# Performance work log

Hardware: AMD Instinct MI355X
Metric: run time of the kernel (lower is better)

The kernel has to match this reference:

```python
import jax, jax.numpy as jnp
import numpy as np

C = 768
HEADS = 12

def setup_inputs() -> dict:
    key = jax.random.key(0)
    k1, k2, k3 = jax.random.split(key, 3)
    x = jax.random.normal(k1, (8, C, 32, 32), dtype=jnp.float32)
    # 1x1 convs are channel-wise linear maps; store as [out_c, in_c]
    w_qkv = jax.random.normal(k2, (3 * C, C), dtype=jnp.float32) * (C ** -0.5)
    w_proj = jax.random.normal(k3, (C, C), dtype=jnp.float32) * (C ** -0.5)
    return {"x": x, "w_qkv": w_qkv, "w_proj": w_proj}

def reference(x, w_qkv, w_proj):
    b, c, h, w = x.shape
    heads = HEADS
    dh = c // heads
    n = h * w
    scale = dh ** -0.5
    # 1x1 conv QKV: [b, 3c, h, w] -> [b, 3, heads, dh, n]
    qkv = jnp.einsum('oc,bchw->bohw', w_qkv, x).reshape(b, 3, heads, dh, n)
    q, k, v = qkv[:, 0], qkv[:, 1], qkv[:, 2]  # each [b, heads, dh, n]
    attn = jnp.einsum('bhdn,bhdm->bhnm', q, k) * scale  # [b, heads, n, n]
    attn = jax.nn.softmax(attn, axis=-1)
    out = jnp.einsum('bhnm,bhdm->bhdn', attn, v)  # [b, heads, dh, n]
    out = out.reshape(b, c, h, w)
    return jnp.einsum('oc,bchw->bohw', w_proj, out)
```

## Files before the change

### kernel.cpp

```cpp
#include <hip/hip_runtime.h>

typedef unsigned short u16;
typedef unsigned int u32;
typedef float v4f __attribute__((ext_vector_type(4)));
typedef __bf16 bf16x8 __attribute__((ext_vector_type(8)));

#define BATCH 8
#define CDIM 768
#define NHEAD 12
#define DH 64
#define NSEQ 1024
#define SCL 0.18033688011112042f

__device__ __forceinline__ u16 f2bf(float f) {
  u32 u = __builtin_bit_cast(u32, f);
  u += 0x7fffu + ((u >> 16) & 1u);
  return (u16)(u >> 16);
}

__device__ __forceinline__ u16 b16(float f) {
  return (u16)((__builtin_bit_cast(u32, f) + 0x8000u) >> 16);
}

__device__ __forceinline__ u32 pkbf(float hi, float lo) {
  u32 a = __builtin_bit_cast(u32, hi) + 0x8000u;
  u32 b = __builtin_bit_cast(u32, lo) + 0x8000u;
  return __builtin_amdgcn_perm(a, b, 0x07060302u);
}

__device__ __forceinline__ v4f mfma16(bf16x8 a, bf16x8 b, v4f c) {
  return __builtin_amdgcn_mfma_f32_16x16x32_bf16(a, b, c, 0, 0, 0);
}

__device__ __forceinline__ void gload16(const u16* g, u16* l) {
  __builtin_amdgcn_global_load_lds(
      (const __attribute__((address_space(1))) void*)g,
      (__attribute__((address_space(3))) void*)l, 16, 0, 0);
}

__global__ __launch_bounds__(256) void k_prep(const float* __restrict__ x,
                                              const float* __restrict__ wq,
                                              const float* __restrict__ wp,
                                              u16* __restrict__ xT,
                                              u16* __restrict__ wqb,
                                              u16* __restrict__ wpb) {
  __shared__ u16 Ts[64][72];
  int bid = blockIdx.x;
  int t = threadIdx.x;
  if (bid < 2304) {
    bool isQ = bid < 1728;
    const float* s = isQ ? wq : wp;
    u16* d = isQ ? wqb : wpb;
    int i = (isQ ? bid : bid - 1728) * 256 + t;
    float4 v = ((const float4*)s)[i];
    u32 lo = (u32)f2bf(v.x) | ((u32)f2bf(v.y) << 16);
    u32 hi = (u32)f2bf(v.z) | ((u32)f2bf(v.w) << 16);
    ((uint2*)d)[i] = uint2{lo, hi};
    return;
  }
  int id = bid - 2304;
  int p0 = (id & 15) * 64; id >>= 4;
  int c0 = (id % 12) * 64; int b = id / 12;
  int cr = t >> 4;
  int p4 = (t & 15) * 4;
  const float* src = x + ((size_t)b * CDIM + c0) * NSEQ + p0;
#pragma unroll
  for (int i = 0; i < 4; ++i) {
    int c = cr + i * 16;
    float4 v = *(const float4*)&src[(size_t)c * NSEQ + p4];
    Ts[p4 + 0][c] = f2bf(v.x);
    Ts[p4 + 1][c] = f2bf(v.y);
    Ts[p4 + 2][c] = f2bf(v.z);
    Ts[p4 + 3][c] = f2bf(v.w);
  }
  __syncthreads();
  int p = t >> 2;
  int cq = t & 3;
  u16* dst = xT + ((size_t)b * NSEQ + p0 + p) * CDIM + c0;
#pragma unroll
  for (int j = 0; j < 2; ++j) {
    int ch = cq + j * 4;
    *(int4*)&dst[ch * 8] = *(const int4*)&Ts[p][ch * 8];
  }
}

#define NKT 24

__device__ __forceinline__ void gemm_core(const u16* __restrict__ Ag,
                                          const u16* __restrict__ Bg,
                                          u16* sm, v4f (&acc)[8][4]) {
  int t = threadIdx.x, lane = t & 63, wid = t >> 6;
  int ln = lane & 15, quad = lane >> 4;
  int wm = wid >> 1, wn = wid & 1;

  int srow = wid * 16 + (lane >> 2);
  int scg = ((lane & 3) ^ ((lane >> 3) & 3)) * 8;
  const u16* As0 = Ag + (size_t)srow * CDIM + scg;
  const u16* Bs0 = Bg + (size_t)srow * CDIM + scg;
  int ldw = wid * 512;

  int cA = (quad ^ ((ln >> 1) & 3)) * 8;
  int rA = (wm * 128 + ln) * 32;
  int rB = 8192 + (wn * 64 + ln) * 32;

  {
    u16* sb0 = sm;
    gload16(As0, sb0 + ldw);
    gload16(As0 + (size_t)64 * CDIM, sb0 + 2048 + ldw);
    gload16(As0 + (size_t)128 * CDIM, sb0 + 4096 + ldw);
    gload16(As0 + (size_t)192 * CDIM, sb0 + 6144 + ldw);
    gload16(Bs0, sb0 + 8192 + ldw);
    gload16(Bs0 + (size_t)64 * CDIM, sb0 + 10240 + ldw);
  }
  asm volatile("" ::: "memory");
  {
    u16* sb1 = sm + 12288;
    gload16(As0 + 32, sb1 + ldw);
    gload16(As0 + (size_t)64 * CDIM + 32, sb1 + 2048 + ldw);
    gload16(As0 + (size_t)128 * CDIM + 32, sb1 + 4096 + ldw);
    gload16(As0 + (size_t)192 * CDIM + 32, sb1 + 6144 + ldw);
    gload16(Bs0 + 32, sb1 + 8192 + ldw);
    gload16(Bs0 + (size_t)64 * CDIM + 32, sb1 + 10240 + ldw);
  }
  asm volatile("s_waitcnt vmcnt(6)" ::: "memory");
  asm volatile("s_barrier" ::: "memory");

  for (int kb = 0; kb < 8; ++kb) {
#pragma unroll
    for (int u = 0; u < 3; ++u) {
      int kt = kb * 3 + u;
      const u16* sb = sm + u * 12288;
      u16* nb = sm + ((u + 2) % 3) * 12288;
      int ko = (kt + 2) * 32;

      bf16x8 af[4], bfr[4];
#pragma unroll
      for (int m = 0; m < 4; ++m)
        af[m] = *(const bf16x8*)&sb[rA + m * 512 + cA];
#pragma unroll
      for (int n = 0; n < 4; ++n)
        bfr[n] = *(const bf16x8*)&sb[rB + n * 512 + cA];
      if (kt < NKT - 2) {
        gload16(As0 + ko, nb + ldw);
        gload16(As0 + (size_t)64 * CDIM + ko, nb + 2048 + ldw);
        gload16(Bs0 + ko, nb + 8192 + ldw);
      }
      asm volatile("s_barrier" ::: "memory");
      asm volatile("s_waitcnt lgkmcnt(0)" ::: "memory");
      __builtin_amdgcn_sched_barrier(0);
      __builtin_amdgcn_s_setprio(1);
#pragma unroll
      for (int m = 0; m < 4; ++m)
#pragma unroll
        for (int n = 0; n < 4; ++n)
          acc[m][n] = mfma16(af[m], bfr[n], acc[m][n]);
      __builtin_amdgcn_s_setprio(0);
      asm volatile("s_barrier" ::: "memory");

#pragma unroll
      for (int m = 0; m < 4; ++m)
        af[m] = *(const bf16x8*)&sb[rA + (m + 4) * 512 + cA];
      if (kt < NKT - 2) {
        gload16(As0 + (size_t)128 * CDIM + ko, nb + 4096 + ldw);
        gload16(As0 + (size_t)192 * CDIM + ko, nb + 6144 + ldw);
        gload16(Bs0 + (size_t)64 * CDIM + ko, nb + 10240 + ldw);
        asm volatile("s_waitcnt vmcnt(6)" ::: "memory");
      } else if (kt == NKT - 2) {
        asm volatile("s_waitcnt vmcnt(0)" ::: "memory");
      }
      asm volatile("s_barrier" ::: "memory");
      asm volatile("s_waitcnt lgkmcnt(0)" ::: "memory");
      __builtin_amdgcn_sched_barrier(0);
      __builtin_amdgcn_s_setprio(1);
#pragma unroll
      for (int m = 0; m < 4; ++m)
#pragma unroll
        for (int n = 0; n < 4; ++n)
          acc[m + 4][n] = mfma16(af[m], bfr[n], acc[m + 4][n]);
      __builtin_amdgcn_s_setprio(0);
      asm volatile("s_barrier" ::: "memory");
    }
  }
}

__global__ __launch_bounds__(256, 2) void k_gemm_qkv(const u16* __restrict__ Wb,
                                                     const u16* __restrict__ xT,
                                                     u16* __restrict__ qkT,
                                                     u16* __restrict__ vbuf) {
  __shared__ u16 sm[3 * 12288];
  int bid = blockIdx.x;
  int swz = (bid & 7) * 72 + (bid >> 3);
  int oIdx = swz % 9, pIdx = swz / 9;
  int oT = oIdx * 256;
  int pG = pIdx * 128;

  v4f acc[8][4] = {};
  gemm_core(Wb + (size_t)oT * CDIM, xT + (size_t)pG * CDIM, sm, acc);

  int t = threadIdx.x, lane = t & 63, wid = t >> 6;
  int ln = lane & 15, quad = lane >> 4;
  int wm = wid >> 1, wn = wid & 1;
  bool isV = oT >= 2 * CDIM;
#pragma unroll
  for (int m = 0; m < 8; ++m) {
#pragma unroll
    for (int n = 0; n < 4; ++n) {
      int ro = oT + wm * 128 + m * 16 + quad * 4;
      int cp = pG + wn * 64 + n * 16 + ln;
      int b = cp >> 10, p = cp & 1023;
      if (!isV) {
        u32 lo = (u32)f2bf(acc[m][n][0]) | ((u32)f2bf(acc[m][n][1]) << 16);
        u32 hi = (u32)f2bf(acc[m][n][2]) | ((u32)f2bf(acc[m][n][3]) << 16);
        *(uint2*)&qkT[((size_t)b * NSEQ + p) * 1536 + ro] = uint2{lo, hi};
      } else {
#pragma unroll
        for (int r = 0; r < 4; ++r)
          vbuf[((size_t)b * CDIM + (ro - 2 * CDIM + r)) * NSEQ + p] =
              f2bf(acc[m][n][r]);
      }
    }
  }
}

__global__ __launch_bounds__(256) void k_attn(const u16* __restrict__ qkT,
                                              const u16* __restrict__ vbuf,
                                              u16* __restrict__ attnT) {
  int id = blockIdx.x;
  int b = id & 7;
  int j = id >> 3;
  int h = j % 12;
  int nt0 = (j / 12) * 128;

  int t = threadIdx.x, lane = t & 63, wid = t >> 6;
  int ln = lane & 15, quad = lane >> 4;
  int nbase = nt0 + wid * 32;

  __shared__ u16 Ks[2][64 * 64];
  __shared__ u16 Vs[2][64 * 64];
  __shared__ u16 Pa[4][32 * 72];
  u16* myP = Pa[wid];

  const u16* qbase = qkT + ((size_t)b * NSEQ + nbase) * 1536 + h * DH;
  bf16x8 aq[2][2];
#pragma unroll
  for (int mt = 0; mt < 2; ++mt)
#pragma unroll
    for (int ks = 0; ks < 2; ++ks)
      aq[mt][ks] = *(const bf16x8*)&qbase[(size_t)(mt * 16 + ln) * 1536 + ks * 32 + quad * 8];

  bf16x8 ones;
#pragma unroll
  for (int i = 0; i < 8; ++i) ones[i] = __builtin_bit_cast(__bf16, (u16)0x3F80);

  v4f oacc[2][4] = {};
  v4f lacc[2] = {};

  int sr8 = lane >> 3;
  int sch = ((lane & 7) ^ sr8) * 8;
  const u16* kg0 = qkT + ((size_t)b * NSEQ + wid * 16 + sr8) * 1536 + CDIM + h * DH + sch;
  const u16* vg0 = vbuf + ((size_t)b * CDIM + h * DH + wid * 16 + sr8) * NSEQ + sch;
  int sK = (wid * 16) * 64;

  int sw0 = (quad ^ (ln & 7)) * 8;
  int sw1 = ((4 + quad) ^ (ln & 7)) * 8;

  gload16(kg0, &Ks[0][sK]);
  gload16(kg0 + (size_t)8 * 1536, &Ks[0][sK + 512]);
  gload16(vg0, &Vs[0][sK]);
  gload16(vg0 + 8 * NSEQ, &Vs[0][sK + 512]);
  __syncthreads();

  for (int s = 0; s < 16; ++s) {
    int cur = s & 1, nxt = cur ^ 1;
    if (s < 15) {
      size_t ko = (size_t)(s + 1) * 64 * 1536;
      int vo = (s + 1) * 64;
      gload16(kg0 + ko, &Ks[nxt][sK]);
      gload16(kg0 + ko + (size_t)8 * 1536, &Ks[nxt][sK + 512]);
      gload16(vg0 + vo, &Vs[nxt][sK]);
      gload16(vg0 + vo + 8 * NSEQ, &Vs[nxt][sK + 512]);
    }

#pragma unroll
    for (int ct = 0; ct < 4; ++ct) {
      bf16x8 kf0 = *(const bf16x8*)&Ks[cur][(ct * 16 + ln) * 64 + sw0];
      bf16x8 kf1 = *(const bf16x8*)&Ks[cur][(ct * 16 + ln) * 64 + sw1];
#pragma unroll
      for (int mt = 0; mt < 2; ++mt) {
        v4f sc = {};
        sc = mfma16(kf0, aq[mt][0], sc);
        sc = mfma16(kf1, aq[mt][1], sc);
        float p0 = __builtin_amdgcn_exp2f(sc[0] * SCL);
        float p1 = __builtin_amdgcn_exp2f(sc[1] * SCL);
        float p2 = __builtin_amdgcn_exp2f(sc[2] * SCL);
        float p3 = __builtin_amdgcn_exp2f(sc[3] * SCL);
        *(uint2*)&myP[(mt * 16 + ln) * 72 + ct * 16 + quad * 4] =
            uint2{pkbf(p1, p0), pkbf(p3, p2)};
      }
    }

    bf16x8 ap[2][2];
#pragma unroll
    for (int mt = 0; mt < 2; ++mt)
#pragma unroll
      for (int ks = 0; ks < 2; ++ks)
        ap[mt][ks] = *(const bf16x8*)&myP[(mt * 16 + ln) * 72 + ks * 32 + quad * 8];
#pragma unroll
    for (int mt = 0; mt < 2; ++mt) {
      lacc[mt] = mfma16(ap[mt][0], ones, lacc[mt]);
      lacc[mt] = mfma16(ap[mt][1], ones, lacc[mt]);
    }
#pragma unroll
    for (int nt = 0; nt < 4; ++nt) {
      bf16x8 vf0 = *(const bf16x8*)&Vs[cur][(nt * 16 + ln) * 64 + sw0];
      bf16x8 vf1 = *(const bf16x8*)&Vs[cur][(nt * 16 + ln) * 64 + sw1];
#pragma unroll
      for (int mt = 0; mt < 2; ++mt) {
        oacc[mt][nt] = mfma16(ap[mt][0], vf0, oacc[mt][nt]);
        oacc[mt][nt] = mfma16(ap[mt][1], vf1, oacc[mt][nt]);
      }
    }
    __syncthreads();
  }

#pragma unroll
  for (int mt = 0; mt < 2; ++mt) {
#pragma unroll
    for (int r = 0; r < 4; ++r) {
      float inv = 1.0f / lacc[mt][r];
      int n = nbase + mt * 16 + quad * 4 + r;
      u16* dst = attnT + ((size_t)b * NSEQ + n) * CDIM + h * DH;
#pragma unroll
      for (int nt = 0; nt < 4; ++nt)
        dst[nt * 16 + ln] = b16(oacc[mt][nt][r] * inv);
    }
  }
}

__global__ __launch_bounds__(256, 2) void k_gemm_proj(const u16* __restrict__ Wb,
                                                      const u16* __restrict__ aT,
                                                      float* __restrict__ out) {
  __shared__ u16 sm[3 * 12288];
  int bid = blockIdx.x;
  int swz = (bid & 7) * 24 + (bid >> 3);
  int oIdx = swz % 3, pIdx = swz / 3;
  int oT = oIdx * 256;
  int pG = pIdx * 128;

  v4f acc[8][4] = {};
  gemm_core(Wb + (size_t)oT * CDIM, aT + (size_t)pG * CDIM, sm, acc);

  int t = threadIdx.x, lane = t & 63, wid = t >> 6;
  int ln = lane & 15, quad = lane >> 4;
  int wm = wid >> 1, wn = wid & 1;
#pragma unroll
  for (int m = 0; m < 8; ++m) {
#pragma unroll
    for (int n = 0; n < 4; ++n) {
      int ro = oT + wm * 128 + m * 16 + quad * 4;
      int cp = pG + wn * 64 + n * 16 + ln;
      int b = cp >> 10, p = cp & 1023;
#pragma unroll
      for (int r = 0; r < 4; ++r)
        out[((size_t)b * CDIM + ro + r) * NSEQ + p] = acc[m][n][r];
    }
  }
}

extern "C" void kernel_launch(void* const* d_in, const int* in_sizes, int n_in,
                              void* d_out, int out_size, void* d_ws, size_t ws_size,
                              hipStream_t stream) {
  const float* x = (const float*)d_in[0];
  const float* w_qkv = (const float*)d_in[1];
  const float* w_proj = (const float*)d_in[2];
  float* out = (float*)d_out;

  char* ws = (char*)d_ws;
  u16* wqkv_bf = (u16*)(ws);
  u16* wproj_bf = (u16*)(ws + 3538944);
  u16* xT = (u16*)(ws + 4718592);
  u16* vbuf = (u16*)(ws + 17301504);
  u16* qkT = (u16*)d_out;
  u16* attnT = xT;

  k_prep<<<dim3(3840), dim3(256), 0, stream>>>(x, w_qkv, w_proj, xT, wqkv_bf, wproj_bf);
  k_gemm_qkv<<<dim3(576), dim3(256), 0, stream>>>(wqkv_bf, xT, qkT, vbuf);
  k_attn<<<dim3(768), dim3(256), 0, stream>>>(qkT, vbuf, attnT);
  k_gemm_proj<<<dim3(192), dim3(256), 0, stream>>>(wproj_bf, attnT, out);
}
```

Measured before the change: 184.6 us.

## Enlarge GEMM tiles to 256x256 with 8 waves and double-buffered 64-wide K stages

The shared QKV/projection GEMM core moves from a 256x128 tile with 4 waves and a triple-buffered 32-wide K pipeline to a 256x256 tile with 8 waves. It now double-buffers 64-wide K stages (two 32-wide sub-slabs each) and interleaves the global-to-LDS loads with MFMA phases through new macros. The goal is more data reuse per loaded tile and fewer K iterations. The cost is 128KB of LDS per block, which allows at most one block per CU. Grid sizes halve to 288 and 96 blocks, so the projection GEMM may leave many CUs idle.

```diff
diff --git a/kernel.cpp b/kernel.cpp
--- a/kernel.cpp
+++ b/kernel.cpp
@@ -84,122 +84,97 @@
   }
 }
 
-#define NKT 24
+#define NIT 6
+
+#define STAGE(gp, db, isB, ks, kt) do {                                   \
+    u16* Ld_ = sm + (db) * 32768 + (isB) * 16384 + (ks) * 8192 + ldw;     \
+    const u16* Gp_ = (gp) + (size_t)(kt) * 64 + (ks) * 32;                \
+    gload16(Gp_, Ld_);                                                    \
+    gload16(Gp_ + (size_t)128 * CDIM, Ld_ + 4096);                        \
+  } while (0)
+
+#define PHASE(db, ks, mh, ...) do {                                       \
+    const u16* Ab_ = sm + (db) * 32768 + (ks) * 8192;                     \
+    const u16* Bb_ = Ab_ + 16384;                                         \
+    bf16x8 af[4];                                                         \
+    _Pragma("unroll") for (int m = 0; m < 4; ++m)                         \
+      af[m] = *(const bf16x8*)&Ab_[rAr + (mh) * 2048 + m * 512 + slot];   \
+    if ((mh) == 0) {                                                      \
+      _Pragma("unroll") for (int n = 0; n < 4; ++n)                       \
+        bfr[n] = *(const bf16x8*)&Bb_[rBr + n * 512 + slot];              \
+    }                                                                     \
+    __VA_ARGS__;                                                          \
+    asm volatile("s_barrier" ::: "memory");                               \
+    asm volatile("s_waitcnt lgkmcnt(0)" ::: "memory");                    \
+    __builtin_amdgcn_sched_barrier(0);                                    \
+    __builtin_amdgcn_s_setprio(1);                                        \
+    _Pragma("unroll") for (int m = 0; m < 4; ++m)                         \
+      _Pragma("unroll") for (int n = 0; n < 4; ++n)                       \
+        acc[(mh) * 4 + m][n] = mfma16(af[m], bfr[n], acc[(mh) * 4 + m][n]); \
+    __builtin_amdgcn_s_setprio(0);                                        \
+    __builtin_amdgcn_sched_barrier(0);                                    \
+    asm volatile("s_barrier" ::: "memory");                               \
+  } while (0)
+
+#define VM4 asm volatile("s_waitcnt vmcnt(4)" ::: "memory")
+#define VM0 asm volatile("s_waitcnt vmcnt(0)" ::: "memory")
+#define FEN asm volatile("" ::: "memory")
 
 __device__ __forceinline__ void gemm_core(const u16* __restrict__ Ag,
                                           const u16* __restrict__ Bg,
                                           u16* sm, v4f (&acc)[8][4]) {
   int t = threadIdx.x, lane = t & 63, wid = t >> 6;
   int ln = lane & 15, quad = lane >> 4;
-  int wm = wid >> 1, wn = wid & 1;
-
-  int srow = wid * 16 + (lane >> 2);
-  int scg = ((lane & 3) ^ ((lane >> 3) & 3)) * 8;
-  const u16* As0 = Ag + (size_t)srow * CDIM + scg;
-  const u16* Bs0 = Bg + (size_t)srow * CDIM + scg;
+  int wm = wid >> 2, wn = wid & 3;
+
+  const u16* As = Ag + (size_t)(t >> 2) * CDIM + ((t & 3) ^ ((t >> 3) & 3)) * 8;
+  const u16* Bs = Bg + (size_t)(t >> 2) * CDIM + ((t & 3) ^ ((t >> 3) & 3)) * 8;
   int ldw = wid * 512;
 
-  int cA = (quad ^ ((ln >> 1) & 3)) * 8;
-  int rA = (wm * 128 + ln) * 32;
-  int rB = 8192 + (wn * 64 + ln) * 32;
-
-  {
-    u16* sb0 = sm;
-    gload16(As0, sb0 + ldw);
-    gload16(As0 + (size_t)64 * CDIM, sb0 + 2048 + ldw);
-    gload16(As0 + (size_t)128 * CDIM, sb0 + 4096 + ldw);
-    gload16(As0 + (size_t)192 * CDIM, sb0 + 6144 + ldw);
-    gload16(Bs0, sb0 + 8192 + ldw);
-    gload16(Bs0 + (size_t)64 * CDIM, sb0 + 10240 + ldw);
-  }
-  asm volatile("" ::: "memory");
-  {
-    u16* sb1 = sm + 12288;
-    gload16(As0 + 32, sb1 + ldw);
-    gload16(As0 + (size_t)64 * CDIM + 32, sb1 + 2048 + ldw);
-    gload16(As0 + (size_t)128 * CDIM + 32, sb1 + 4096 + ldw);
-    gload16(As0 + (size_t)192 * CDIM + 32, sb1 + 6144 + ldw);
-    gload16(Bs0 + 32, sb1 + 8192 + ldw);
-    gload16(Bs0 + (size_t)64 * CDIM + 32, sb1 + 10240 + ldw);
-  }
-  asm volatile("s_waitcnt vmcnt(6)" ::: "memory");
+  int slot = (quad ^ ((ln >> 1) & 3)) * 8;
+  int rAr = (wm * 128 + ln) * 32;
+  int rBr = (wn * 64 + ln) * 32;
+
+  bf16x8 bfr[4];
+
+  STAGE(As, 0, 0, 0, 0); FEN;
+  STAGE(Bs, 0, 1, 0, 0); FEN;
+  STAGE(As, 0, 0, 1, 0); FEN;
+  STAGE(Bs, 0, 1, 1, 0);
+  VM4;
   asm volatile("s_barrier" ::: "memory");
 
-  for (int kb = 0; kb < 8; ++kb) {
-#pragma unroll
-    for (int u = 0; u < 3; ++u) {
-      int kt = kb * 3 + u;
-      const u16* sb = sm + u * 12288;
-      u16* nb = sm + ((u + 2) % 3) * 12288;
-      int ko = (kt + 2) * 32;
-
-      bf16x8 af[4], bfr[4];
-#pragma unroll
-      for (int m = 0; m < 4; ++m)
-        af[m] = *(const bf16x8*)&sb[rA + m * 512 + cA];
-#pragma unroll
-      for (int n = 0; n < 4; ++n)
-        bfr[n] = *(const bf16x8*)&sb[rB + n * 512 + cA];
-      if (kt < NKT - 2) {
-        gload16(As0 + ko, nb + ldw);
-        gload16(As0 + (size_t)64 * CDIM + ko, nb + 2048 + ldw);
-        gload16(Bs0 + ko, nb + 8192 + ldw);
-      }
-      asm volatile("s_barrier" ::: "memory");
-      asm volatile("s_waitcnt lgkmcnt(0)" ::: "memory");
-      __builtin_amdgcn_sched_barrier(0);
-      __builtin_amdgcn_s_setprio(1);
-#pragma unroll
-      for (int m = 0; m < 4; ++m)
-#pragma unroll
-        for (int n = 0; n < 4; ++n)
-          acc[m][n] = mfma16(af[m], bfr[n], acc[m][n]);
-      __builtin_amdgcn_s_setprio(0);
-      asm volatile("s_barrier" ::: "memory");
-
-#pragma unroll
-      for (int m = 0; m < 4; ++m)
-        af[m] = *(const bf16x8*)&sb[rA + (m + 4) * 512 + cA];
-      if (kt < NKT - 2) {
-        gload16(As0 + (size_t)128 * CDIM + ko, nb + 4096 + ldw);
-        gload16(As0 + (size_t)192 * CDIM + ko, nb + 6144 + ldw);
-        gload16(Bs0 + (size_t)64 * CDIM + ko, nb + 10240 + ldw);
-        asm volatile("s_waitcnt vmcnt(6)" ::: "memory");
-      } else if (kt == NKT - 2) {
-        asm volatile("s_waitcnt vmcnt(0)" ::: "memory");
-      }
-      asm volatile("s_barrier" ::: "memory");
-      asm volatile("s_waitcnt lgkmcnt(0)" ::: "memory");
-      __builtin_amdgcn_sched_barrier(0);
-      __builtin_amdgcn_s_setprio(1);
-#pragma unroll
-      for (int m = 0; m < 4; ++m)
-#pragma unroll
-        for (int n = 0; n < 4; ++n)
-          acc[m + 4][n] = mfma16(af[m], bfr[n], acc[m + 4][n]);
-      __builtin_amdgcn_s_setprio(0);
-      asm volatile("s_barrier" ::: "memory");
-    }
-  }
-}
-
-__global__ __launch_bounds__(256, 2) void k_gemm_qkv(const u16* __restrict__ Wb,
+  for (int i = 0; i < NIT; ++i) {
+    int b = 2 * i + 1, n2 = 2 * i + 2;
+    bool nl = (i < NIT - 1);
+    PHASE(0, 0, 0, STAGE(As, 1, 0, 0, b));
+    PHASE(0, 0, 1, STAGE(Bs, 1, 1, 0, b); VM4);
+    PHASE(0, 1, 0, STAGE(As, 1, 0, 1, b));
+    PHASE(0, 1, 1, STAGE(Bs, 1, 1, 1, b); VM4);
+    PHASE(1, 0, 0, if (nl) STAGE(As, 0, 0, 0, n2));
+    PHASE(1, 0, 1, if (nl) { STAGE(Bs, 0, 1, 0, n2); VM4; } else { VM0; });
+    PHASE(1, 1, 0, if (nl) STAGE(As, 0, 0, 1, n2));
+    PHASE(1, 1, 1, if (nl) { STAGE(Bs, 0, 1, 1, n2); VM4; });
+  }
+}
+
+__global__ __launch_bounds__(512, 2) void k_gemm_qkv(const u16* __restrict__ Wb,
                                                      const u16* __restrict__ xT,
                                                      u16* __restrict__ qkT,
                                                      u16* __restrict__ vbuf) {
-  __shared__ u16 sm[3 * 12288];
+  __shared__ u16 sm[65536];
   int bid = blockIdx.x;
-  int swz = (bid & 7) * 72 + (bid >> 3);
+  int swz = (bid & 7) * 36 + (bid >> 3);
   int oIdx = swz % 9, pIdx = swz / 9;
   int oT = oIdx * 256;
-  int pG = pIdx * 128;
+  int pG = pIdx * 256;
 
   v4f acc[8][4] = {};
   gemm_core(Wb + (size_t)oT * CDIM, xT + (size_t)pG * CDIM, sm, acc);
 
   int t = threadIdx.x, lane = t & 63, wid = t >> 6;
   int ln = lane & 15, quad = lane >> 4;
-  int wm = wid >> 1, wn = wid & 1;
+  int wm = wid >> 2, wn = wid & 3;
   bool isV = oT >= 2 * CDIM;
 #pragma unroll
   for (int m = 0; m < 8; ++m) {
@@ -337,22 +312,22 @@
   }
 }
 
-__global__ __launch_bounds__(256, 2) void k_gemm_proj(const u16* __restrict__ Wb,
+__global__ __launch_bounds__(512, 2) void k_gemm_proj(const u16* __restrict__ Wb,
                                                       const u16* __restrict__ aT,
                                                       float* __restrict__ out) {
-  __shared__ u16 sm[3 * 12288];
+  __shared__ u16 sm[65536];
   int bid = blockIdx.x;
-  int swz = (bid & 7) * 24 + (bid >> 3);
+  int swz = (bid & 7) * 12 + (bid >> 3);
   int oIdx = swz % 3, pIdx = swz / 3;
   int oT = oIdx * 256;
-  int pG = pIdx * 128;
+  int pG = pIdx * 256;
 
   v4f acc[8][4] = {};
   gemm_core(Wb + (size_t)oT * CDIM, aT + (size_t)pG * CDIM, sm, acc);
 
   int t = threadIdx.x, lane = t & 63, wid = t >> 6;
   int ln = lane & 15, quad = lane >> 4;
-  int wm = wid >> 1, wn = wid & 1;
+  int wm = wid >> 2, wn = wid & 3;
 #pragma unroll
   for (int m = 0; m < 8; ++m) {
 #pragma unroll
@@ -384,7 +359,7 @@
   u16* attnT = xT;
 
   k_prep<<<dim3(3840), dim3(256), 0, stream>>>(x, w_qkv, w_proj, xT, wqkv_bf, wproj_bf);
-  k_gemm_qkv<<<dim3(576), dim3(256), 0, stream>>>(wqkv_bf, xT, qkT, vbuf);
+  k_gemm_qkv<<<dim3(288), dim3(512), 0, stream>>>(wqkv_bf, xT, qkT, vbuf);
   k_attn<<<dim3(768), dim3(256), 0, stream>>>(qkT, vbuf, attnT);
-  k_gemm_proj<<<dim3(192), dim3(256), 0, stream>>>(wproj_bf, attnT, out);
-}
+  k_gemm_proj<<<dim3(96), dim3(512), 0, stream>>>(wproj_bf, attnT, out);
+}
```

Measured after the change: 198.0 us. 7.3% more time.

## Switch GEMM core to double-buffered LDS and raise occupancy to 3 blocks

Applied to the files above, without the earlier changes.

Replaces the triple-buffered shared-memory pipeline in the shared GEMM core with a double-buffered one that prefetches one k-tile ahead, and rebalances which tile rows are loaded in each half-iteration. The reduced LDS footprint lets launch bounds rise to three blocks per CU for the QKV and projection GEMMs. This trades prefetch depth for occupancy, which may expose more memory latency and tightens the register budget for the large accumulator array.

```diff
diff --git a/kernel.cpp b/kernel.cpp
--- a/kernel.cpp
+++ b/kernel.cpp
@@ -104,90 +104,81 @@
   int rB = 8192 + (wn * 64 + ln) * 32;
 
   {
-    u16* sb0 = sm;
-    gload16(As0, sb0 + ldw);
-    gload16(As0 + (size_t)64 * CDIM, sb0 + 2048 + ldw);
-    gload16(As0 + (size_t)128 * CDIM, sb0 + 4096 + ldw);
-    gload16(As0 + (size_t)192 * CDIM, sb0 + 6144 + ldw);
-    gload16(Bs0, sb0 + 8192 + ldw);
-    gload16(Bs0 + (size_t)64 * CDIM, sb0 + 10240 + ldw);
+    u16* s0 = sm;
+    gload16(As0, s0 + ldw);
+    gload16(As0 + (size_t)128 * CDIM, s0 + 4096 + ldw);
+    gload16(Bs0, s0 + 8192 + ldw);
+    gload16(Bs0 + (size_t)64 * CDIM, s0 + 10240 + ldw);
   }
   asm volatile("" ::: "memory");
   {
-    u16* sb1 = sm + 12288;
-    gload16(As0 + 32, sb1 + ldw);
-    gload16(As0 + (size_t)64 * CDIM + 32, sb1 + 2048 + ldw);
-    gload16(As0 + (size_t)128 * CDIM + 32, sb1 + 4096 + ldw);
-    gload16(As0 + (size_t)192 * CDIM + 32, sb1 + 6144 + ldw);
-    gload16(Bs0 + 32, sb1 + 8192 + ldw);
-    gload16(Bs0 + (size_t)64 * CDIM + 32, sb1 + 10240 + ldw);
-  }
-  asm volatile("s_waitcnt vmcnt(6)" ::: "memory");
+    u16* s0 = sm;
+    gload16(As0 + (size_t)64 * CDIM, s0 + 2048 + ldw);
+    gload16(As0 + (size_t)192 * CDIM, s0 + 6144 + ldw);
+  }
+  asm volatile("s_waitcnt vmcnt(2)" ::: "memory");
   asm volatile("s_barrier" ::: "memory");
 
-  for (int kb = 0; kb < 8; ++kb) {
-#pragma unroll
-    for (int u = 0; u < 3; ++u) {
-      int kt = kb * 3 + u;
-      const u16* sb = sm + u * 12288;
-      u16* nb = sm + ((u + 2) % 3) * 12288;
-      int ko = (kt + 2) * 32;
-
-      bf16x8 af[4], bfr[4];
-#pragma unroll
-      for (int m = 0; m < 4; ++m)
-        af[m] = *(const bf16x8*)&sb[rA + m * 512 + cA];
+  for (int kt = 0; kt < NKT; ++kt) {
+    const u16* sb = sm + (kt & 1) * 12288;
+    u16* nb = sm + ((kt + 1) & 1) * 12288;
+    int ko = (kt + 1) * 32;
+
+    bf16x8 af[4], bfr[4];
+#pragma unroll
+    for (int m = 0; m < 4; ++m)
+      af[m] = *(const bf16x8*)&sb[rA + m * 512 + cA];
+#pragma unroll
+    for (int n = 0; n < 4; ++n)
+      bfr[n] = *(const bf16x8*)&sb[rB + n * 512 + cA];
+    if (kt < NKT - 1) {
+      gload16(As0 + ko, nb + ldw);
+      gload16(As0 + (size_t)128 * CDIM + ko, nb + 4096 + ldw);
+      gload16(Bs0 + ko, nb + 8192 + ldw);
+      gload16(Bs0 + (size_t)64 * CDIM + ko, nb + 10240 + ldw);
+      asm volatile("s_waitcnt vmcnt(4)" ::: "memory");
+    } else {
+      asm volatile("s_waitcnt vmcnt(0)" ::: "memory");
+    }
+    asm volatile("s_barrier" ::: "memory");
+    asm volatile("s_waitcnt lgkmcnt(0)" ::: "memory");
+    __builtin_amdgcn_sched_barrier(0);
+    __builtin_amdgcn_s_setprio(1);
+#pragma unroll
+    for (int m = 0; m < 4; ++m)
 #pragma unroll
       for (int n = 0; n < 4; ++n)
-        bfr[n] = *(const bf16x8*)&sb[rB + n * 512 + cA];
-      if (kt < NKT - 2) {
-        gload16(As0 + ko, nb + ldw);
-        gload16(As0 + (size_t)64 * CDIM + ko, nb + 2048 + ldw);
-        gload16(Bs0 + ko, nb + 8192 + ldw);
-      }
-      asm volatile("s_barrier" ::: "memory");
-      asm volatile("s_waitcnt lgkmcnt(0)" ::: "memory");
-      __builtin_amdgcn_sched_barrier(0);
-      __builtin_amdgcn_s_setprio(1);
-#pragma unroll
-      for (int m = 0; m < 4; ++m)
-#pragma unroll
-        for (int n = 0; n < 4; ++n)
-          acc[m][n] = mfma16(af[m], bfr[n], acc[m][n]);
-      __builtin_amdgcn_s_setprio(0);
-      asm volatile("s_barrier" ::: "memory");
-
-#pragma unroll
-      for (int m = 0; m < 4; ++m)
-        af[m] = *(const bf16x8*)&sb[rA + (m + 4) * 512 + cA];
-      if (kt < NKT - 2) {
-        gload16(As0 + (size_t)128 * CDIM + ko, nb + 4096 + ldw);
-        gload16(As0 + (size_t)192 * CDIM + ko, nb + 6144 + ldw);
-        gload16(Bs0 + (size_t)64 * CDIM + ko, nb + 10240 + ldw);
-        asm volatile("s_waitcnt vmcnt(6)" ::: "memory");
-      } else if (kt == NKT - 2) {
-        asm volatile("s_waitcnt vmcnt(0)" ::: "memory");
-      }
-      asm volatile("s_barrier" ::: "memory");
-      asm volatile("s_waitcnt lgkmcnt(0)" ::: "memory");
-      __builtin_amdgcn_sched_barrier(0);
-      __builtin_amdgcn_s_setprio(1);
-#pragma unroll
-      for (int m = 0; m < 4; ++m)
-#pragma unroll
-        for (int n = 0; n < 4; ++n)
-          acc[m + 4][n] = mfma16(af[m], bfr[n], acc[m + 4][n]);
-      __builtin_amdgcn_s_setprio(0);
-      asm volatile("s_barrier" ::: "memory");
-    }
-  }
-}
-
-__global__ __launch_bounds__(256, 2) void k_gemm_qkv(const u16* __restrict__ Wb,
+        acc[m][n] = mfma16(af[m], bfr[n], acc[m][n]);
+    __builtin_amdgcn_s_setprio(0);
+    asm volatile("s_barrier" ::: "memory");
+
+#pragma unroll
+    for (int m = 0; m < 4; ++m)
+      af[m] = *(const bf16x8*)&sb[rA + (m + 4) * 512 + cA];
+    if (kt < NKT - 1) {
+      gload16(As0 + (size_t)64 * CDIM + ko, nb + 2048 + ldw);
+      gload16(As0 + (size_t)192 * CDIM + ko, nb + 6144 + ldw);
+      asm volatile("s_waitcnt vmcnt(2)" ::: "memory");
+    }
+    asm volatile("s_barrier" ::: "memory");
+    asm volatile("s_waitcnt lgkmcnt(0)" ::: "memory");
+    __builtin_amdgcn_sched_barrier(0);
+    __builtin_amdgcn_s_setprio(1);
+#pragma unroll
+    for (int m = 0; m < 4; ++m)
+#pragma unroll
+      for (int n = 0; n < 4; ++n)
+        acc[m + 4][n] = mfma16(af[m], bfr[n], acc[m + 4][n]);
+    __builtin_amdgcn_s_setprio(0);
+    asm volatile("s_barrier" ::: "memory");
+  }
+}
+
+__global__ __launch_bounds__(256, 3) void k_gemm_qkv(const u16* __restrict__ Wb,
                                                      const u16* __restrict__ xT,
                                                      u16* __restrict__ qkT,
                                                      u16* __restrict__ vbuf) {
-  __shared__ u16 sm[3 * 12288];
+  __shared__ u16 sm[2 * 12288];
   int bid = blockIdx.x;
   int swz = (bid & 7) * 72 + (bid >> 3);
   int oIdx = swz % 9, pIdx = swz / 9;
@@ -337,10 +328,10 @@
   }
 }
 
-__global__ __launch_bounds__(256, 2) void k_gemm_proj(const u16* __restrict__ Wb,
+__global__ __launch_bounds__(256, 3) void k_gemm_proj(const u16* __restrict__ Wb,
                                                       const u16* __restrict__ aT,
                                                       float* __restrict__ out) {
-  __shared__ u16 sm[3 * 12288];
+  __shared__ u16 sm[2 * 12288];
   int bid = blockIdx.x;
   int swz = (bid & 7) * 24 + (bid >> 3);
   int oIdx = swz % 3, pIdx = swz / 3;
```

Result: slower. 218.7 us (+18.5%).

## Retile QKV GEMM to 288x256 tiles with 8 waves and 256 blocks

Applied to the files above, without the earlier changes.

Replaces the QKV projection GEMM with a standalone kernel that uses 512-thread blocks, 288x256 output tiles and a grid of 256 blocks. That matches one wave of work across the 256 CUs instead of 576 smaller blocks. The load roles are split: six waves stage weight rows and two stage activation rows into a triple-buffered LDS pipeline. Each wave now computes a 144x64 tile (9x4 MFMA blocks), raising arithmetic intensity. The costs are higher register and LDS use per block, and mixed Q/K/V stores inside one tile, since 288 does not divide the 768-row boundaries.

```diff
diff --git a/kernel.cpp b/kernel.cpp
--- a/kernel.cpp
+++ b/kernel.cpp
@@ -37,6 +37,11 @@
       (const __attribute__((address_space(1))) void*)g,
       (__attribute__((address_space(3))) void*)l, 16, 0, 0);
 }
+
+#define BARQ asm volatile("s_barrier" ::: "memory")
+#define LGKM0 asm volatile("s_waitcnt lgkmcnt(0)" ::: "memory")
+#define VMC0 asm volatile("s_waitcnt vmcnt(0)" ::: "memory")
+#define FEN asm volatile("" ::: "memory")
 
 __global__ __launch_bounds__(256) void k_prep(const float* __restrict__ x,
                                               const float* __restrict__ wq,
@@ -86,6 +91,127 @@
 
 #define NKT 24
 
+__global__ __launch_bounds__(512, 2) void k_gemm_qkv(const u16* __restrict__ Wb,
+                                                     const u16* __restrict__ xT,
+                                                     u16* __restrict__ qkT,
+                                                     u16* __restrict__ vbuf) {
+  __shared__ u16 sm[3 * 17408];
+  int bid = blockIdx.x;
+  int swz = (bid & 7) * 32 + (bid >> 3);
+  int oIdx = swz % 8, pIdx = swz / 8;
+  int oT = oIdx * 288;
+  int pG = pIdx * 256;
+
+  int t = threadIdx.x, lane = t & 63, wid = t >> 6;
+  int ln = lane & 15, quad = lane >> 4;
+  int wm = wid >> 2, wn = wid & 3;
+
+  int lrow = lane >> 2;
+  int scg = ((lane & 3) ^ ((lane >> 3) & 3)) * 8;
+  bool roleA = wid < 6;
+  int w6 = wid - 6;
+  const u16* Asrc = Wb + (size_t)(oT + wid * 48 + lrow) * CDIM + scg;
+  const u16* Bsrc = xT + (size_t)(pG + (w6 < 0 ? 0 : w6) * 128 + lrow) * CDIM + scg;
+  int ldA = wid * 1536;
+  int ldB = 9216 + (w6 < 0 ? 0 : w6) * 4096;
+
+#define STAGEQ(bi, kt) do {                                                \
+    u16* bb_ = sm + (bi) * 17408;                                          \
+    if (roleA) {                                                           \
+      const u16* gp_ = Asrc + (kt) * 32;                                   \
+      gload16(gp_, bb_ + ldA);                                             \
+      gload16(gp_ + (size_t)16 * CDIM, bb_ + ldA + 512);                   \
+      gload16(gp_ + (size_t)32 * CDIM, bb_ + ldA + 1024);                  \
+    } else {                                                               \
+      const u16* gp_ = Bsrc + (kt) * 32;                                   \
+      _Pragma("unroll") for (int i_ = 0; i_ < 8; ++i_)                     \
+        gload16(gp_ + (size_t)i_ * 16 * CDIM, bb_ + ldB + i_ * 512);       \
+    }                                                                      \
+  } while (0)
+
+#define DRAINQ do {                                                        \
+    if (roleA) asm volatile("s_waitcnt vmcnt(3)" ::: "memory");            \
+    else asm volatile("s_waitcnt vmcnt(8)" ::: "memory");                  \
+  } while (0)
+
+  int slot = (quad ^ ((ln >> 1) & 3)) * 8;
+  int rAr = (wm * 144 + ln) * 32;
+  int rBr = 9216 + (wn * 64 + ln) * 32;
+
+  v4f acc[9][4] = {};
+
+  STAGEQ(0, 0);
+  FEN;
+  STAGEQ(1, 1);
+  DRAINQ;
+  BARQ;
+
+  for (int j = 0; j < NKT; ++j) {
+    const u16* sb = sm + (j % 3) * 17408;
+    int bi2 = (j + 2) % 3;
+
+    if (j < NKT - 2) STAGEQ(bi2, j + 2);
+    bf16x8 af[5], bfr[4];
+#pragma unroll
+    for (int m = 0; m < 5; ++m)
+      af[m] = *(const bf16x8*)&sb[rAr + m * 512 + slot];
+#pragma unroll
+    for (int n = 0; n < 4; ++n)
+      bfr[n] = *(const bf16x8*)&sb[rBr + n * 512 + slot];
+    BARQ;
+    LGKM0;
+    __builtin_amdgcn_sched_barrier(0);
+    __builtin_amdgcn_s_setprio(1);
+#pragma unroll
+    for (int m = 0; m < 5; ++m)
+#pragma unroll
+      for (int n = 0; n < 4; ++n)
+        acc[m][n] = mfma16(af[m], bfr[n], acc[m][n]);
+    __builtin_amdgcn_s_setprio(0);
+    BARQ;
+
+    bf16x8 ag[4];
+#pragma unroll
+    for (int m = 0; m < 4; ++m)
+      ag[m] = *(const bf16x8*)&sb[rAr + (m + 5) * 512 + slot];
+    if (j < NKT - 2) DRAINQ;
+    else if (j == NKT - 2) VMC0;
+    BARQ;
+    LGKM0;
+    __builtin_amdgcn_sched_barrier(0);
+    __builtin_amdgcn_s_setprio(1);
+#pragma unroll
+    for (int m = 0; m < 4; ++m)
+#pragma unroll
+      for (int n = 0; n < 4; ++n)
+        acc[m + 5][n] = mfma16(ag[m], bfr[n], acc[m + 5][n]);
+    __builtin_amdgcn_s_setprio(0);
+    BARQ;
+  }
+
+#pragma unroll
+  for (int m = 0; m < 9; ++m) {
+#pragma unroll
+    for (int n = 0; n < 4; ++n) {
+      int ro = oT + wm * 144 + m * 16 + quad * 4;
+      int cp = pG + wn * 64 + n * 16 + ln;
+      int b = cp >> 10, p = cp & 1023;
+      if (ro < 2 * CDIM) {
+        u32 lo = (u32)f2bf(acc[m][n][0]) | ((u32)f2bf(acc[m][n][1]) << 16);
+        u32 hi = (u32)f2bf(acc[m][n][2]) | ((u32)f2bf(acc[m][n][3]) << 16);
+        *(uint2*)&qkT[((size_t)b * NSEQ + p) * 1536 + ro] = uint2{lo, hi};
+      } else {
+#pragma unroll
+        for (int r = 0; r < 4; ++r)
+          vbuf[((size_t)b * CDIM + (ro - 2 * CDIM + r)) * NSEQ + p] =
+              f2bf(acc[m][n][r]);
+      }
+    }
+  }
+#undef STAGEQ
+#undef DRAINQ
+}
+
 __device__ __forceinline__ void gemm_core(const u16* __restrict__ Ag,
                                           const u16* __restrict__ Bg,
                                           u16* sm, v4f (&acc)[8][4]) {
@@ -112,7 +238,7 @@
     gload16(Bs0, sb0 + 8192 + ldw);
     gload16(Bs0 + (size_t)64 * CDIM, sb0 + 10240 + ldw);
   }
-  asm volatile("" ::: "memory");
+  FEN;
   {
     u16* sb1 = sm + 12288;
     gload16(As0 + 32, sb1 + ldw);
@@ -123,7 +249,7 @@
     gload16(Bs0 + (size_t)64 * CDIM + 32, sb1 + 10240 + ldw);
   }
   asm volatile("s_waitcnt vmcnt(6)" ::: "memory");
-  asm volatile("s_barrier" ::: "memory");
+  BARQ;
 
   for (int kb = 0; kb < 8; ++kb) {
 #pragma unroll
@@ -145,8 +271,8 @@
         gload16(As0 + (size_t)64 * CDIM + ko, nb + 2048 + ldw);
         gload16(Bs0 + ko, nb + 8192 + ldw);
       }
-      asm volatile("s_barrier" ::: "memory");
-      asm volatile("s_waitcnt lgkmcnt(0)" ::: "memory");
+      BARQ;
+      LGKM0;
       __builtin_amdgcn_sched_barrier(0);
       __builtin_amdgcn_s_setprio(1);
 #pragma unroll
@@ -155,7 +281,7 @@
         for (int n = 0; n < 4; ++n)
           acc[m][n] = mfma16(af[m], bfr[n], acc[m][n]);
       __builtin_amdgcn_s_setprio(0);
-      asm volatile("s_barrier" ::: "memory");
+      BARQ;
 
 #pragma unroll
       for (int m = 0; m < 4; ++m)
@@ -166,10 +292,10 @@
         gload16(Bs0 + (size_t)64 * CDIM + ko, nb + 10240 + ldw);
         asm volatile("s_waitcnt vmcnt(6)" ::: "memory");
       } else if (kt == NKT - 2) {
-        asm volatile("s_waitcnt vmcnt(0)" ::: "memory");
+        VMC0;
       }
-      asm volatile("s_barrier" ::: "memory");
-      asm volatile("s_waitcnt lgkmcnt(0)" ::: "memory");
+      BARQ;
+      LGKM0;
       __builtin_amdgcn_sched_barrier(0);
       __builtin_amdgcn_s_setprio(1);
 #pragma unroll
@@ -178,46 +304,7 @@
         for (int n = 0; n < 4; ++n)
           acc[m + 4][n] = mfma16(af[m], bfr[n], acc[m + 4][n]);
       __builtin_amdgcn_s_setprio(0);
-      asm volatile("s_barrier" ::: "memory");
-    }
-  }
-}
-
-__global__ __launch_bounds__(256, 2) void k_gemm_qkv(const u16* __restrict__ Wb,
-                                                     const u16* __restrict__ xT,
-                                                     u16* __restrict__ qkT,
-                                                     u16* __restrict__ vbuf) {
-  __shared__ u16 sm[3 * 12288];
-  int bid = blockIdx.x;
-  int swz = (bid & 7) * 72 + (bid >> 3);
-  int oIdx = swz % 9, pIdx = swz / 9;
-  int oT = oIdx * 256;
-  int pG = pIdx * 128;
-
-  v4f acc[8][4] = {};
-  gemm_core(Wb + (size_t)oT * CDIM, xT + (size_t)pG * CDIM, sm, acc);
-
-  int t = threadIdx.x, lane = t & 63, wid = t >> 6;
-  int ln = lane & 15, quad = lane >> 4;
-  int wm = wid >> 1, wn = wid & 1;
-  bool isV = oT >= 2 * CDIM;
-#pragma unroll
-  for (int m = 0; m < 8; ++m) {
-#pragma unroll
-    for (int n = 0; n < 4; ++n) {
-      int ro = oT + wm * 128 + m * 16 + quad * 4;
-      int cp = pG + wn * 64 + n * 16 + ln;
-      int b = cp >> 10, p = cp & 1023;
-      if (!isV) {
-        u32 lo = (u32)f2bf(acc[m][n][0]) | ((u32)f2bf(acc[m][n][1]) << 16);
-        u32 hi = (u32)f2bf(acc[m][n][2]) | ((u32)f2bf(acc[m][n][3]) << 16);
-        *(uint2*)&qkT[((size_t)b * NSEQ + p) * 1536 + ro] = uint2{lo, hi};
-      } else {
-#pragma unroll
-        for (int r = 0; r < 4; ++r)
-          vbuf[((size_t)b * CDIM + (ro - 2 * CDIM + r)) * NSEQ + p] =
-              f2bf(acc[m][n][r]);
-      }
+      BARQ;
     }
   }
 }
@@ -384,7 +471,7 @@
   u16* attnT = xT;
 
   k_prep<<<dim3(3840), dim3(256), 0, stream>>>(x, w_qkv, w_proj, xT, wqkv_bf, wproj_bf);
-  k_gemm_qkv<<<dim3(576), dim3(256), 0, stream>>>(wqkv_bf, xT, qkT, vbuf);
+  k_gemm_qkv<<<dim3(256), dim3(512), 0, stream>>>(wqkv_bf, xT, qkT, vbuf);
   k_attn<<<dim3(768), dim3(256), 0, stream>>>(qkT, vbuf, attnT);
   k_gemm_proj<<<dim3(192), dim3(256), 0, stream>>>(wproj_bf, attnT, out);
 }
```

Result: faster. 176.6 us (-4.3%).
